# Optimization experiments

Hardware: AMD Instinct MI355X
Metric: run time of the kernel (lower is better)

Reference implementation:

```python
import jax, jax.numpy as jnp
import numpy as np

IN_CH = 512
OUT_CH = 512
HEADS = 8
HEAD_DIM = OUT_CH // HEADS
N = 64 * 64  # total flattened tokens


def setup_inputs() -> dict:
    key = jax.random.key(0)
    ks = jax.random.split(key, 10)
    x = jax.random.normal(ks[0], (64, 64, IN_CH), dtype=jnp.float32)
    edge_index = jax.random.randint(ks[1], (2, 65536), 0, N, dtype=jnp.int64)
    # causal temporal mask, broadcastable against scores [N, H, N]
    temporal_mask = jnp.tril(jnp.ones((N, N), dtype=bool))[:, None, :]
    s = 1.0 / np.sqrt(IN_CH)
    Wq = jax.random.uniform(ks[2], (OUT_CH, IN_CH), minval=-s, maxval=s)
    bq = jnp.zeros((OUT_CH,), jnp.float32)
    Wk = jax.random.uniform(ks[3], (OUT_CH, IN_CH), minval=-s, maxval=s)
    bk = jnp.zeros((OUT_CH,), jnp.float32)
    Wv = jax.random.uniform(ks[4], (OUT_CH, IN_CH), minval=-s, maxval=s)
    bv = jnp.zeros((OUT_CH,), jnp.float32)
    Wo = jax.random.uniform(ks[5], (OUT_CH, OUT_CH), minval=-s, maxval=s)
    bo = jnp.zeros((OUT_CH,), jnp.float32)
    return {"x": x, "edge_index": edge_index, "temporal_mask": temporal_mask,
            "Wq": Wq, "bq": bq, "Wk": Wk, "bk": bk, "Wv": Wv, "bv": bv,
            "Wo": Wo, "bo": bo}


def reference(x, edge_index, temporal_mask, Wq, bq, Wk, bk, Wv, bv, Wo, bo):
    # x: [S1, S2, C] -> flatten to [N, C]; edge_index unused (as in source).
    xf = x.reshape(-1, IN_CH)
    q = (xf @ Wq.T + bq).reshape(-1, HEADS, HEAD_DIM)
    k = (xf @ Wk.T + bk).reshape(-1, HEADS, HEAD_DIM)
    v = (xf @ Wv.T + bv).reshape(-1, HEADS, HEAD_DIM)
    scores = jnp.einsum('nhd,mhd->nhm', q, k) / np.sqrt(HEAD_DIM)  # [N,H,N]
    scores = jnp.where(temporal_mask, scores, -jnp.inf)
    attn = jax.nn.softmax(scores, axis=-1)  # dropout omitted (eval mode)
    out = jnp.einsum('nhm,mhd->nhd', attn, v).reshape(-1, OUT_CH)
    return out @ Wo.T + bo  # [N, OUT_CH]
```

## Files before the change

kernel.cpp:

```cpp
#include <hip/hip_runtime.h>
#include <math.h>

#define NT 4096
#define CH 512
#define NHEADS 8
#define HD 64

typedef __attribute__((ext_vector_type(8))) short short8;
typedef __attribute__((ext_vector_type(4))) float f32x4;
typedef unsigned short ushort_t;
typedef unsigned int uint_t;

#define MFMA16 __builtin_amdgcn_mfma_f32_16x16x32_bf16

#define MNEG 1e30f

__device__ __forceinline__ ushort_t f2bf(float x) {
  uint_t u = __float_as_uint(x);
  return (ushort_t)((u + 0x7fffu + ((u >> 16) & 1u)) >> 16);
}
__device__ __forceinline__ float bf2f(ushort_t h) {
  return __uint_as_float(((uint_t)h) << 16);
}

__device__ __forceinline__ void g2l16(const ushort_t* g, ushort_t* l) {
  __builtin_amdgcn_global_load_lds(
      (const __attribute__((address_space(1))) void*)g,
      (__attribute__((address_space(3))) void*)l, 16, 0, 0);
}

__device__ __forceinline__ short8 ldsFrag(const ushort_t* plane, int row, int c4) {
  return *reinterpret_cast<const short8*>(plane + row * 64 + (((c4) ^ (row & 7)) << 3));
}

__global__ __launch_bounds__(256)
void cvt_split(const float* __restrict__ x,
               const float* __restrict__ Wq, const float* __restrict__ Wk,
               const float* __restrict__ Wv, const float* __restrict__ Wo,
               ushort_t* __restrict__ xh, ushort_t* __restrict__ xl,
               ushort_t* __restrict__ qh, ushort_t* __restrict__ ql,
               ushort_t* __restrict__ kh, ushort_t* __restrict__ kl,
               ushort_t* __restrict__ vh, ushort_t* __restrict__ vl,
               ushort_t* __restrict__ oh, ushort_t* __restrict__ ol) {
  const size_t i = ((size_t)blockIdx.x * 256 + threadIdx.x) * 4;
  const float* src;
  ushort_t *dh, *dl;
  size_t off;
  if (i < 2097152) { src = x; dh = xh; dl = xl; off = i; }
  else {
    const size_t j = i - 2097152;
    const int wsel = (int)(j >> 18);
    off = j & 262143;
    if (wsel == 0)      { src = Wq; dh = qh; dl = ql; }
    else if (wsel == 1) { src = Wk; dh = kh; dl = kl; }
    else if (wsel == 2) { src = Wv; dh = vh; dl = vl; }
    else                { src = Wo; dh = oh; dl = ol; }
  }
  const float4 v = *reinterpret_cast<const float4*>(src + off);
  ushort_t hb[4], lb[4];
  const float f[4] = {v.x, v.y, v.z, v.w};
  #pragma unroll
  for (int j = 0; j < 4; ++j) {
    hb[j] = f2bf(f[j]);
    lb[j] = f2bf(f[j] - bf2f(hb[j]));
  }
  *reinterpret_cast<uint2*>(dh + off) =
      make_uint2((uint_t)hb[0] | ((uint_t)hb[1] << 16), (uint_t)hb[2] | ((uint_t)hb[3] << 16));
  *reinterpret_cast<uint2*>(dl + off) =
      make_uint2((uint_t)lb[0] | ((uint_t)lb[1] << 16), (uint_t)lb[2] | ((uint_t)lb[3] << 16));
}

__global__ __launch_bounds__(256)
void gemm_qkv_bf16(const ushort_t* __restrict__ xh,
                   const ushort_t* __restrict__ Wqh, const float* __restrict__ bq,
                   const ushort_t* __restrict__ Wkh, const float* __restrict__ bk,
                   const ushort_t* __restrict__ Wvh, const float* __restrict__ bv,
                   ushort_t* __restrict__ Qhi, ushort_t* __restrict__ Khi,
                   ushort_t* __restrict__ Vthi) {
  __shared__ ushort_t ldsA[128 * 64];
  __shared__ ushort_t ldsW[64 * 64];
  const int z = blockIdx.z;
  const ushort_t* Wh = (z == 0) ? Wqh : (z == 1) ? Wkh : Wvh;
  const float* bias = (z == 0) ? bq : (z == 1) ? bk : bv;

  const int t = threadIdx.x;
  const int w = t >> 6;
  const int lane = t & 63;
  const int l15 = lane & 15;
  const int g = lane >> 4;
  const int m0 = blockIdx.x * 128;
  const int n0 = blockIdx.y * 64;

  f32x4 acc[2][4];
  #pragma unroll
  for (int mt = 0; mt < 2; ++mt)
    #pragma unroll
    for (int nt = 0; nt < 4; ++nt) acc[mt][nt] = f32x4{0.f, 0.f, 0.f, 0.f};

  for (int k0 = 0; k0 < 512; k0 += 64) {
    __syncthreads();
    #pragma unroll
    for (int p = 0; p < 4; ++p) {
      const int c = 256 * p + 64 * w + lane;
      const int r = c >> 3;
      const int sc4 = (c & 7) ^ (r & 7);
      g2l16(xh + (size_t)(m0 + r) * 512 + k0 + sc4 * 8,
            &ldsA[(256 * p + 64 * w) * 8]);
    }
    #pragma unroll
    for (int p = 0; p < 2; ++p) {
      const int c = 256 * p + 64 * w + lane;
      const int r = c >> 3;
      const int sc4 = (c & 7) ^ (r & 7);
      g2l16(Wh + (size_t)(n0 + r) * 512 + k0 + sc4 * 8,
            &ldsW[(256 * p + 64 * w) * 8]);
    }
    __syncthreads();
    #pragma unroll
    for (int s = 0; s < 2; ++s) {
      short8 ah[2];
      #pragma unroll
      for (int mt = 0; mt < 2; ++mt)
        ah[mt] = ldsFrag(ldsA, 32 * w + 16 * mt + l15, 4 * s + g);
      #pragma unroll
      for (int nt = 0; nt < 4; ++nt) {
        const short8 wh = ldsFrag(ldsW, 16 * nt + l15, 4 * s + g);
        #pragma unroll
        for (int mt = 0; mt < 2; ++mt)
          acc[mt][nt] = MFMA16(ah[mt], wh, acc[mt][nt], 0, 0, 0);
      }
    }
  }

  if (z < 2) {
    ushort_t* Hi = z ? Khi : Qhi;
    const float sc = z ? 1.0f : 0.125f;
    #pragma unroll
    for (int mt = 0; mt < 2; ++mt) {
      const int mb = m0 + 32 * w + 16 * mt + 4 * g;
      #pragma unroll
      for (int nt = 0; nt < 4; ++nt) {
        const int col = n0 + 16 * nt + l15;
        const float bv_ = bias[col];
        #pragma unroll
        for (int r = 0; r < 4; ++r)
          Hi[(size_t)(mb + r) * 512 + col] = f2bf((acc[mt][nt][r] + bv_) * sc);
      }
    }
  } else {
    #pragma unroll
    for (int mt = 0; mt < 2; ++mt) {
      const int mb = m0 + 32 * w + 16 * mt + 4 * g;
      #pragma unroll
      for (int nt = 0; nt < 4; ++nt) {
        const int n = n0 + 16 * nt + l15;
        const float bv_ = bias[n];
        ushort_t hb[4];
        #pragma unroll
        for (int r = 0; r < 4; ++r) hb[r] = f2bf(acc[mt][nt][r] + bv_);
        *reinterpret_cast<uint2*>(&Vthi[(size_t)n * 4096 + mb]) =
            make_uint2((uint_t)hb[0] | ((uint_t)hb[1] << 16),
                       (uint_t)hb[2] | ((uint_t)hb[3] << 16));
      }
    }
  }
}

__global__ __launch_bounds__(256)
void gemm_out_mfma(const ushort_t* __restrict__ Ahi, const ushort_t* __restrict__ Alo,
                   const ushort_t* __restrict__ Woh, const ushort_t* __restrict__ Wol,
                   const float* __restrict__ bias, float* __restrict__ C) {
  __shared__ ushort_t ldsAh[128 * 64], ldsAl[128 * 64];
  __shared__ ushort_t ldsWh[64 * 64], ldsWl[64 * 64];
  const int t = threadIdx.x;
  const int w = t >> 6;
  const int lane = t & 63;
  const int l15 = lane & 15;
  const int g = lane >> 4;
  const int m0 = blockIdx.x * 128;
  const int n0 = blockIdx.y * 64;

  f32x4 acc[2][4];
  #pragma unroll
  for (int mt = 0; mt < 2; ++mt)
    #pragma unroll
    for (int nt = 0; nt < 4; ++nt) acc[mt][nt] = f32x4{0.f, 0.f, 0.f, 0.f};

  for (int k0 = 0; k0 < 512; k0 += 64) {
    __syncthreads();
    #pragma unroll
    for (int p = 0; p < 4; ++p) {
      const int c = 256 * p + 64 * w + lane;
      const int r = c >> 3;
      const int sc4 = (c & 7) ^ (r & 7);
      const size_t src = (size_t)(m0 + r) * 512 + k0 + sc4 * 8;
      const int dst = (256 * p + 64 * w) * 8;
      g2l16(Ahi + src, ldsAh + dst);
      g2l16(Alo + src, ldsAl + dst);
    }
    #pragma unroll
    for (int p = 0; p < 2; ++p) {
      const int c = 256 * p + 64 * w + lane;
      const int r = c >> 3;
      const int sc4 = (c & 7) ^ (r & 7);
      const size_t src = (size_t)(n0 + r) * 512 + k0 + sc4 * 8;
      const int dst = (256 * p + 64 * w) * 8;
      g2l16(Woh + src, ldsWh + dst);
      g2l16(Wol + src, ldsWl + dst);
    }
    __syncthreads();
    #pragma unroll
    for (int s = 0; s < 2; ++s) {
      short8 ah[2], al[2];
      #pragma unroll
      for (int mt = 0; mt < 2; ++mt) {
        ah[mt] = ldsFrag(ldsAh, 32 * w + 16 * mt + l15, 4 * s + g);
        al[mt] = ldsFrag(ldsAl, 32 * w + 16 * mt + l15, 4 * s + g);
      }
      #pragma unroll
      for (int nt = 0; nt < 4; ++nt) {
        const short8 wh = ldsFrag(ldsWh, 16 * nt + l15, 4 * s + g);
        const short8 wl = ldsFrag(ldsWl, 16 * nt + l15, 4 * s + g);
        #pragma unroll
        for (int mt = 0; mt < 2; ++mt) {
          acc[mt][nt] = MFMA16(ah[mt], wh, acc[mt][nt], 0, 0, 0);
          acc[mt][nt] = MFMA16(ah[mt], wl, acc[mt][nt], 0, 0, 0);
          acc[mt][nt] = MFMA16(al[mt], wh, acc[mt][nt], 0, 0, 0);
        }
      }
    }
  }

  #pragma unroll
  for (int mt = 0; mt < 2; ++mt) {
    const int mb = m0 + 32 * w + 16 * mt + 4 * g;
    #pragma unroll
    for (int nt = 0; nt < 4; ++nt) {
      const int col = n0 + 16 * nt + l15;
      const float bv_ = bias[col];
      #pragma unroll
      for (int r = 0; r < 4; ++r)
        C[(size_t)(mb + r) * 512 + col] = acc[mt][nt][r] + bv_;
    }
  }
}

__global__ __launch_bounds__(512)
void attn_mfma(const ushort_t* __restrict__ Qhi, const ushort_t* __restrict__ Khi,
               const ushort_t* __restrict__ Vthi,
               float* __restrict__ Opart, float2* __restrict__ MLpart) {
  __shared__ ushort_t ldsT[2][64 * 64];
  __shared__ ushort_t ldsP[8][16 * 64];

  const int t = threadIdx.x;
  const int h = blockIdx.y;
  const int w = t >> 6;
  const int lane = t & 63;
  const int l15 = lane & 15;
  const int g = lane >> 4;

  const int bx = blockIdx.x;
  const int qb = 31 - bx / 3;
  const int sp = bx - 3 * (bx / 3);
  const int ntiles = 2 * qb + 2;
  const int len = (ntiles + 2) / 3;
  const int kb0 = sp * len;
  const int kb1e = (kb0 + len < ntiles) ? (kb0 + len) : ntiles;
  const int q0 = qb * 128;
  const int qr = q0 + w * 16 + l15;

  const short8 ones = {(short)0x3F80, (short)0x3F80, (short)0x3F80, (short)0x3F80,
                       (short)0x3F80, (short)0x3F80, (short)0x3F80, (short)0x3F80};

  short8 qh[2];
  #pragma unroll
  for (int s = 0; s < 2; ++s)
    qh[s] = *reinterpret_cast<const short8*>(
        Qhi + (size_t)qr * 512 + h * 64 + 32 * s + 8 * g);

  float mrun[4], lrun[4];
  f32x4 accO[4];
  #pragma unroll
  for (int r = 0; r < 4; ++r) { mrun[r] = -MNEG; lrun[r] = 0.f; }
  #pragma unroll
  for (int dt = 0; dt < 4; ++dt) accO[dt] = f32x4{0.f, 0.f, 0.f, 0.f};

  for (int kb = kb0; kb < kb1e; ++kb) {
    __syncthreads();
    {
      const int c = w * 64 + lane;
      const int r = c >> 3;
      const int sc4 = (c & 7) ^ (r & 7);
      const int ldst = (w * 64) * 8;
      g2l16(Khi + (size_t)(kb * 64 + r) * 512 + h * 64 + sc4 * 8, &ldsT[0][ldst]);
      g2l16(Vthi + (size_t)(h * 64 + r) * 4096 + kb * 64 + sc4 * 8, &ldsT[1][ldst]);
    }
    __syncthreads();

    f32x4 accS[4];
    #pragma unroll
    for (int nt = 0; nt < 4; ++nt) accS[nt] = f32x4{0.f, 0.f, 0.f, 0.f};
    __builtin_amdgcn_s_setprio(1);
    #pragma unroll
    for (int s = 0; s < 2; ++s) {
      #pragma unroll
      for (int nt = 0; nt < 4; ++nt) {
        const short8 kh = ldsFrag(ldsT[0], 16 * nt + l15, 4 * s + g);
        accS[nt] = MFMA16(qh[s], kh, accS[nt], 0, 0, 0);
      }
    }
    __builtin_amdgcn_s_setprio(0);

    if (kb >= 2 * qb) {
      #pragma unroll
      for (int nt = 0; nt < 4; ++nt) {
        const int kg = kb * 64 + 16 * nt + l15;
        #pragma unroll
        for (int r = 0; r < 4; ++r) {
          const int qg = q0 + w * 16 + 4 * g + r;
          if (kg > qg) accS[nt][r] = -INFINITY;
        }
      }
    }

    float pmax[4];
    #pragma unroll
    for (int r = 0; r < 4; ++r)
      pmax[r] = fmaxf(fmaxf(accS[0][r], accS[1][r]), fmaxf(accS[2][r], accS[3][r]));
    float dd = pmax[0] - mrun[0];
    #pragma unroll
    for (int r = 1; r < 4; ++r) dd = fmaxf(dd, pmax[r] - mrun[r]);
    if (!__all(dd <= 8.0f)) {
      #pragma unroll
      for (int off = 1; off < 16; off <<= 1)
        #pragma unroll
        for (int r = 0; r < 4; ++r) pmax[r] = fmaxf(pmax[r], __shfl_xor(pmax[r], off));
      #pragma unroll
      for (int r = 0; r < 4; ++r) {
        const float mn = fmaxf(mrun[r], pmax[r]);
        const float al = __expf(mrun[r] - mn);
        mrun[r] = mn;
        lrun[r] *= al;
        #pragma unroll
        for (int dt = 0; dt < 4; ++dt) accO[dt][r] *= al;
      }
    }
    #pragma unroll
    for (int nt = 0; nt < 4; ++nt)
      #pragma unroll
      for (int r = 0; r < 4; ++r) {
        const float p = __expf(accS[nt][r] - mrun[r]);
        const int row = 4 * g + r;
        ldsP[w][row * 64 + (((2 * nt + (l15 >> 3)) ^ (row & 7)) << 3) + (l15 & 7)]
            = f2bf(p);
      }
    short8 pah[2];
    #pragma unroll
    for (int s = 0; s < 2; ++s) pah[s] = ldsFrag(ldsP[w], l15, 4 * s + g);

    f32x4 accL = f32x4{0.f, 0.f, 0.f, 0.f};
    __builtin_amdgcn_s_setprio(1);
    #pragma unroll
    for (int s = 0; s < 2; ++s) {
      accL = MFMA16(pah[s], ones, accL, 0, 0, 0);
      #pragma unroll
      for (int dt = 0; dt < 4; ++dt) {
        const short8 vh = ldsFrag(ldsT[1], 16 * dt + l15, 4 * s + g);
        accO[dt] = MFMA16(pah[s], vh, accO[dt], 0, 0, 0);
      }
    }
    __builtin_amdgcn_s_setprio(0);
    #pragma unroll
    for (int r = 0; r < 4; ++r) lrun[r] += accL[r];
  }

  #pragma unroll
  for (int r = 0; r < 4; ++r) {
    const int rw = w * 16 + 4 * g + r;
    const size_t pbase = ((((size_t)sp * 32 + qb) * 8 + h) * 128 + rw) * 64;
    #pragma unroll
    for (int dt = 0; dt < 4; ++dt)
      Opart[pbase + 16 * dt + l15] = accO[dt][r];
    if (l15 == 0)
      MLpart[(((size_t)sp * 32 + qb) * 8 + h) * 128 + rw] = make_float2(mrun[r], lrun[r]);
  }
}

__global__ __launch_bounds__(512)
void attn_combine(const float* __restrict__ Opart, const float2* __restrict__ MLpart,
                  ushort_t* __restrict__ Ahi, ushort_t* __restrict__ Alo) {
  const int qb = blockIdx.x;
  const int h = blockIdx.y;
  const int t = threadIdx.x;
  const int row = t >> 2;
  const int c0 = (t & 3) * 16;
  const size_t mlidx = (((size_t)qb) * 8 + h) * 128 + row;
  const size_t SPS = (size_t)32 * 8 * 128;
  const float2 ml0 = MLpart[mlidx];
  const float2 ml1 = MLpart[mlidx + SPS];
  const float2 ml2 = MLpart[mlidx + 2 * SPS];
  const float M = fmaxf(fmaxf(ml0.x, ml1.x), ml2.x);
  const float w0 = __expf(ml0.x - M);
  const float w1 = __expf(ml1.x - M);
  const float w2 = __expf(ml2.x - M);
  const float inv = 1.0f / (w0 * ml0.y + w1 * ml1.y + w2 * ml2.y);
  const size_t b0 = mlidx * 64;
  const size_t b1 = (mlidx + SPS) * 64;
  const size_t b2 = (mlidx + 2 * SPS) * 64;
  #pragma unroll
  for (int p = 0; p < 4; ++p) {
    const int col = c0 + p * 4;
    const float4 o0 = *reinterpret_cast<const float4*>(&Opart[b0 + col]);
    const float4 o1 = *reinterpret_cast<const float4*>(&Opart[b1 + col]);
    const float4 o2 = *reinterpret_cast<const float4*>(&Opart[b2 + col]);
    const float f[4] = {o0.x * w0 + o1.x * w1 + o2.x * w2,
                        o0.y * w0 + o1.y * w1 + o2.y * w2,
                        o0.z * w0 + o1.z * w1 + o2.z * w2,
                        o0.w * w0 + o1.w * w1 + o2.w * w2};
    ushort_t hb[4], lb[4];
    #pragma unroll
    for (int j = 0; j < 4; ++j) {
      const float v = f[j] * inv;
      hb[j] = f2bf(v);
      lb[j] = f2bf(v - bf2f(hb[j]));
    }
    const size_t idx = (size_t)(qb * 128 + row) * 512 + h * 64 + col;
    *reinterpret_cast<uint2*>(&Ahi[idx]) =
        make_uint2((uint_t)hb[0] | ((uint_t)hb[1] << 16), (uint_t)hb[2] | ((uint_t)hb[3] << 16));
    *reinterpret_cast<uint2*>(&Alo[idx]) =
        make_uint2((uint_t)lb[0] | ((uint_t)lb[1] << 16), (uint_t)lb[2] | ((uint_t)lb[3] << 16));
  }
}

extern "C" void kernel_launch(void* const* d_in, const int* in_sizes, int n_in,
                              void* d_out, int out_size, void* d_ws, size_t ws_size,
                              hipStream_t stream) {
  const float* x  = (const float*)d_in[0];
  const float* Wq = (const float*)d_in[3];
  const float* bq = (const float*)d_in[4];
  const float* Wk = (const float*)d_in[5];
  const float* bk = (const float*)d_in[6];
  const float* Wv = (const float*)d_in[7];
  const float* bv = (const float*)d_in[8];
  const float* Wo = (const float*)d_in[9];
  const float* bo = (const float*)d_in[10];
  float* out = (float*)d_out;

  ushort_t* p = (ushort_t*)d_ws;
  const size_t NC = (size_t)NT * CH;
  const size_t WW = (size_t)CH * CH;
  ushort_t* xhi = p;            p += NC;
  ushort_t* xlo = p;            p += NC;
  ushort_t* Wqh = p;            p += WW;
  ushort_t* Wql = p;            p += WW;
  ushort_t* Wkh = p;            p += WW;
  ushort_t* Wkl = p;            p += WW;
  ushort_t* Wvh = p;            p += WW;
  ushort_t* Wvl = p;            p += WW;
  ushort_t* Woh = p;            p += WW;
  ushort_t* Wol = p;            p += WW;
  ushort_t* Qhi = p;            p += NC;
  ushort_t* Khi = p;            p += NC;
  ushort_t* Vthi = p;           p += NC;
  ushort_t* Ahi = p;            p += NC;
  ushort_t* Alo = p;            p += NC;
  float* Opart = (float*)p;
  float2* MLpart = (float2*)(Opart + 6291456);

  cvt_split<<<3072, 256, 0, stream>>>(x, Wq, Wk, Wv, Wo,
                                      xhi, xlo, Wqh, Wql, Wkh, Wkl, Wvh, Wvl, Woh, Wol);
  gemm_qkv_bf16<<<dim3(32, 8, 3), 256, 0, stream>>>(
      xhi, Wqh, bq, Wkh, bk, Wvh, bv, Qhi, Khi, Vthi);
  attn_mfma<<<dim3(96, 8), 512, 0, stream>>>(Qhi, Khi, Vthi, Opart, MLpart);
  attn_combine<<<dim3(32, 8), 512, 0, stream>>>(Opart, MLpart, Ahi, Alo);
  gemm_out_mfma<<<dim3(32, 8), 256, 0, stream>>>(Ahi, Alo, Woh, Wol, bo, out);
}
```

Baseline: 99.40 us.

## Drop split-bf16 low parts and widen attention key tiles to 128

Removes the hi/lo bf16 split everywhere: conversion writes only the high part, the combine kernel stops emitting Alo, and the output GEMM runs a single bf16 MFMA pass instead of three. The attention kernel now processes 128-key tiles instead of 64, with separate K and V LDS buffers and wider P staging, which halves loop iterations and barriers. Both changes cut memory traffic and MFMA work, at the cost of lower output-projection precision and more LDS per block.

Result: slower. 102.6 us (+3.2%).

```diff
diff --git a/kernel.cpp b/kernel.cpp
--- a/kernel.cpp
+++ b/kernel.cpp
@@ -32,42 +32,75 @@
 __device__ __forceinline__ short8 ldsFrag(const ushort_t* plane, int row, int c4) {
   return *reinterpret_cast<const short8*>(plane + row * 64 + (((c4) ^ (row & 7)) << 3));
 }
+__device__ __forceinline__ short8 ldsFrag128(const ushort_t* plane, int row, int c4) {
+  return *reinterpret_cast<const short8*>(plane + row * 128 + (((c4) ^ (row & 7)) << 3));
+}
 
 __global__ __launch_bounds__(256)
-void cvt_split(const float* __restrict__ x,
-               const float* __restrict__ Wq, const float* __restrict__ Wk,
-               const float* __restrict__ Wv, const float* __restrict__ Wo,
-               ushort_t* __restrict__ xh, ushort_t* __restrict__ xl,
-               ushort_t* __restrict__ qh, ushort_t* __restrict__ ql,
-               ushort_t* __restrict__ kh, ushort_t* __restrict__ kl,
-               ushort_t* __restrict__ vh, ushort_t* __restrict__ vl,
-               ushort_t* __restrict__ oh, ushort_t* __restrict__ ol) {
+void cvt_hi(const float* __restrict__ x,
+            const float* __restrict__ Wq, const float* __restrict__ Wk,
+            const float* __restrict__ Wv, const float* __restrict__ Wo,
+            ushort_t* __restrict__ xh, ushort_t* __restrict__ qh,
+            ushort_t* __restrict__ kh, ushort_t* __restrict__ vh,
+            ushort_t* __restrict__ oh) {
   const size_t i = ((size_t)blockIdx.x * 256 + threadIdx.x) * 4;
   const float* src;
-  ushort_t *dh, *dl;
+  ushort_t* dh;
   size_t off;
-  if (i < 2097152) { src = x; dh = xh; dl = xl; off = i; }
+  if (i < 2097152) { src = x; dh = xh; off = i; }
   else {
     const size_t j = i - 2097152;
     const int wsel = (int)(j >> 18);
     off = j & 262143;
-    if (wsel == 0)      { src = Wq; dh = qh; dl = ql; }
-    else if (wsel == 1) { src = Wk; dh = kh; dl = kl; }
-    else if (wsel == 2) { src = Wv; dh = vh; dl = vl; }
-    else                { src = Wo; dh = oh; dl = ol; }
+    if (wsel == 0)      { src = Wq; dh = qh; }
+    else if (wsel == 1) { src = Wk; dh = kh; }
+    else if (wsel == 2) { src = Wv; dh = vh; }
+    else                { src = Wo; dh = oh; }
   }
   const float4 v = *reinterpret_cast<const float4*>(src + off);
-  ushort_t hb[4], lb[4];
-  const float f[4] = {v.x, v.y, v.z, v.w};
-  #pragma unroll
-  for (int j = 0; j < 4; ++j) {
-    hb[j] = f2bf(f[j]);
-    lb[j] = f2bf(f[j] - bf2f(hb[j]));
-  }
+  const ushort_t hb[4] = {f2bf(v.x), f2bf(v.y), f2bf(v.z), f2bf(v.w)};
   *reinterpret_cast<uint2*>(dh + off) =
       make_uint2((uint_t)hb[0] | ((uint_t)hb[1] << 16), (uint_t)hb[2] | ((uint_t)hb[3] << 16));
-  *reinterpret_cast<uint2*>(dl + off) =
-      make_uint2((uint_t)lb[0] | ((uint_t)lb[1] << 16), (uint_t)lb[2] | ((uint_t)lb[3] << 16));
+}
+
+__device__ __forceinline__ void gemm_hi_core(
+    const ushort_t* __restrict__ Ah, const ushort_t* __restrict__ Wh,
+    int m0, int n0, int w, int lane, ushort_t* ldsA, ushort_t* ldsW,
+    f32x4 acc[2][4]) {
+  const int l15 = lane & 15;
+  const int g = lane >> 4;
+  for (int k0 = 0; k0 < 512; k0 += 64) {
+    __syncthreads();
+    #pragma unroll
+    for (int p = 0; p < 4; ++p) {
+      const int c = 256 * p + 64 * w + lane;
+      const int r = c >> 3;
+      const int sc4 = (c & 7) ^ (r & 7);
+      g2l16(Ah + (size_t)(m0 + r) * 512 + k0 + sc4 * 8, &ldsA[(256 * p + 64 * w) * 8]);
+    }
+    #pragma unroll
+    for (int p = 0; p < 2; ++p) {
+      const int c = 256 * p + 64 * w + lane;
+      const int r = c >> 3;
+      const int sc4 = (c & 7) ^ (r & 7);
+      g2l16(Wh + (size_t)(n0 + r) * 512 + k0 + sc4 * 8, &ldsW[(256 * p + 64 * w) * 8]);
+    }
+    __syncthreads();
+    #pragma unroll
+    for (int s = 0; s < 2; ++s) {
+      short8 ah[2];
+      #pragma unroll
+      for (int mt = 0; mt < 2; ++mt)
+        ah[mt] = ldsFrag(ldsA, 32 * w + 16 * mt + l15, 4 * s + g);
+      #pragma unroll
+      for (int nt = 0; nt < 4; ++nt) {
+        const short8 wh = ldsFrag(ldsW, 16 * nt + l15, 4 * s + g);
+        #pragma unroll
+        for (int mt = 0; mt < 2; ++mt)
+          acc[mt][nt] = MFMA16(ah[mt], wh, acc[mt][nt], 0, 0, 0);
+      }
+    }
+  }
 }
 
 __global__ __launch_bounds__(256)
@@ -97,40 +130,7 @@
     #pragma unroll
     for (int nt = 0; nt < 4; ++nt) acc[mt][nt] = f32x4{0.f, 0.f, 0.f, 0.f};
 
-  for (int k0 = 0; k0 < 512; k0 += 64) {
-    __syncthreads();
-    #pragma unroll
-    for (int p = 0; p < 4; ++p) {
-      const int c = 256 * p + 64 * w + lane;
-      const int r = c >> 3;
-      const int sc4 = (c & 7) ^ (r & 7);
-      g2l16(xh + (size_t)(m0 + r) * 512 + k0 + sc4 * 8,
-            &ldsA[(256 * p + 64 * w) * 8]);
-    }
-    #pragma unroll
-    for (int p = 0; p < 2; ++p) {
-      const int c = 256 * p + 64 * w + lane;
-      const int r = c >> 3;
-      const int sc4 = (c & 7) ^ (r & 7);
-      g2l16(Wh + (size_t)(n0 + r) * 512 + k0 + sc4 * 8,
-            &ldsW[(256 * p + 64 * w) * 8]);
-    }
-    __syncthreads();
-    #pragma unroll
-    for (int s = 0; s < 2; ++s) {
-      short8 ah[2];
-      #pragma unroll
-      for (int mt = 0; mt < 2; ++mt)
-        ah[mt] = ldsFrag(ldsA, 32 * w + 16 * mt + l15, 4 * s + g);
-      #pragma unroll
-      for (int nt = 0; nt < 4; ++nt) {
-        const short8 wh = ldsFrag(ldsW, 16 * nt + l15, 4 * s + g);
-        #pragma unroll
-        for (int mt = 0; mt < 2; ++mt)
-          acc[mt][nt] = MFMA16(ah[mt], wh, acc[mt][nt], 0, 0, 0);
-      }
-    }
-  }
+  gemm_hi_core(xh, Wh, m0, n0, w, lane, ldsA, ldsW, acc);
 
   if (z < 2) {
     ushort_t* Hi = z ? Khi : Qhi;
@@ -167,11 +167,10 @@
 }
 
 __global__ __launch_bounds__(256)
-void gemm_out_mfma(const ushort_t* __restrict__ Ahi, const ushort_t* __restrict__ Alo,
-                   const ushort_t* __restrict__ Woh, const ushort_t* __restrict__ Wol,
+void gemm_out_bf16(const ushort_t* __restrict__ Ahi, const ushort_t* __restrict__ Woh,
                    const float* __restrict__ bias, float* __restrict__ C) {
-  __shared__ ushort_t ldsAh[128 * 64], ldsAl[128 * 64];
-  __shared__ ushort_t ldsWh[64 * 64], ldsWl[64 * 64];
+  __shared__ ushort_t ldsA[128 * 64];
+  __shared__ ushort_t ldsW[64 * 64];
   const int t = threadIdx.x;
   const int w = t >> 6;
   const int lane = t & 63;
@@ -186,50 +185,7 @@
     #pragma unroll
     for (int nt = 0; nt < 4; ++nt) acc[mt][nt] = f32x4{0.f, 0.f, 0.f, 0.f};
 
-  for (int k0 = 0; k0 < 512; k0 += 64) {
-    __syncthreads();
-    #pragma unroll
-    for (int p = 0; p < 4; ++p) {
-      const int c = 256 * p + 64 * w + lane;
-      const int r = c >> 3;
-      const int sc4 = (c & 7) ^ (r & 7);
-      const size_t src = (size_t)(m0 + r) * 512 + k0 + sc4 * 8;
-      const int dst = (256 * p + 64 * w) * 8;
-      g2l16(Ahi + src, ldsAh + dst);
-      g2l16(Alo + src, ldsAl + dst);
-    }
-    #pragma unroll
-    for (int p = 0; p < 2; ++p) {
-      const int c = 256 * p + 64 * w + lane;
-      const int r = c >> 3;
-      const int sc4 = (c & 7) ^ (r & 7);
-      const size_t src = (size_t)(n0 + r) * 512 + k0 + sc4 * 8;
-      const int dst = (256 * p + 64 * w) * 8;
-      g2l16(Woh + src, ldsWh + dst);
-      g2l16(Wol + src, ldsWl + dst);
-    }
-    __syncthreads();
-    #pragma unroll
-    for (int s = 0; s < 2; ++s) {
-      short8 ah[2], al[2];
-      #pragma unroll
-      for (int mt = 0; mt < 2; ++mt) {
-        ah[mt] = ldsFrag(ldsAh, 32 * w + 16 * mt + l15, 4 * s + g);
-        al[mt] = ldsFrag(ldsAl, 32 * w + 16 * mt + l15, 4 * s + g);
-      }
-      #pragma unroll
-      for (int nt = 0; nt < 4; ++nt) {
-        const short8 wh = ldsFrag(ldsWh, 16 * nt + l15, 4 * s + g);
-        const short8 wl = ldsFrag(ldsWl, 16 * nt + l15, 4 * s + g);
-        #pragma unroll
-        for (int mt = 0; mt < 2; ++mt) {
-          acc[mt][nt] = MFMA16(ah[mt], wh, acc[mt][nt], 0, 0, 0);
-          acc[mt][nt] = MFMA16(ah[mt], wl, acc[mt][nt], 0, 0, 0);
-          acc[mt][nt] = MFMA16(al[mt], wh, acc[mt][nt], 0, 0, 0);
-        }
-      }
-    }
-  }
+  gemm_hi_core(Ahi, Woh, m0, n0, w, lane, ldsA, ldsW, acc);
 
   #pragma unroll
   for (int mt = 0; mt < 2; ++mt) {
@@ -249,8 +205,9 @@
 void attn_mfma(const ushort_t* __restrict__ Qhi, const ushort_t* __restrict__ Khi,
                const ushort_t* __restrict__ Vthi,
                float* __restrict__ Opart, float2* __restrict__ MLpart) {
-  __shared__ ushort_t ldsT[2][64 * 64];
-  __shared__ ushort_t ldsP[8][16 * 64];
+  __shared__ ushort_t ldsK[128 * 64];
+  __shared__ ushort_t ldsV[64 * 128];
+  __shared__ ushort_t ldsP[8][16 * 128];
 
   const int t = threadIdx.x;
   const int h = blockIdx.y;
@@ -262,7 +219,7 @@
   const int bx = blockIdx.x;
   const int qb = 31 - bx / 3;
   const int sp = bx - 3 * (bx / 3);
-  const int ntiles = 2 * qb + 2;
+  const int ntiles = qb + 1;
   const int len = (ntiles + 2) / 3;
   const int kb0 = sp * len;
   const int kb1e = (kb0 + len < ntiles) ? (kb0 + len) : ntiles;
@@ -287,34 +244,38 @@
 
   for (int kb = kb0; kb < kb1e; ++kb) {
     __syncthreads();
-    {
-      const int c = w * 64 + lane;
-      const int r = c >> 3;
-      const int sc4 = (c & 7) ^ (r & 7);
-      const int ldst = (w * 64) * 8;
-      g2l16(Khi + (size_t)(kb * 64 + r) * 512 + h * 64 + sc4 * 8, &ldsT[0][ldst]);
-      g2l16(Vthi + (size_t)(h * 64 + r) * 4096 + kb * 64 + sc4 * 8, &ldsT[1][ldst]);
+    #pragma unroll
+    for (int p = 0; p < 2; ++p) {
+      const int ck = p * 512 + w * 64 + lane;
+      const int rk = ck >> 3;
+      const int sck = (ck & 7) ^ (rk & 7);
+      g2l16(Khi + (size_t)(kb * 128 + rk) * 512 + h * 64 + sck * 8,
+            &ldsK[(p * 512 + w * 64) * 8]);
+      const int rv = ck >> 4;
+      const int scv = (ck & 15) ^ (rv & 7);
+      g2l16(Vthi + (size_t)(h * 64 + rv) * 4096 + kb * 128 + scv * 8,
+            &ldsV[(p * 512 + w * 64) * 8]);
     }
     __syncthreads();
 
-    f32x4 accS[4];
-    #pragma unroll
-    for (int nt = 0; nt < 4; ++nt) accS[nt] = f32x4{0.f, 0.f, 0.f, 0.f};
+    f32x4 accS[8];
+    #pragma unroll
+    for (int nt = 0; nt < 8; ++nt) accS[nt] = f32x4{0.f, 0.f, 0.f, 0.f};
     __builtin_amdgcn_s_setprio(1);
     #pragma unroll
     for (int s = 0; s < 2; ++s) {
       #pragma unroll
-      for (int nt = 0; nt < 4; ++nt) {
-        const short8 kh = ldsFrag(ldsT[0], 16 * nt + l15, 4 * s + g);
+      for (int nt = 0; nt < 8; ++nt) {
+        const short8 kh = ldsFrag(ldsK, 16 * nt + l15, 4 * s + g);
         accS[nt] = MFMA16(qh[s], kh, accS[nt], 0, 0, 0);
       }
     }
     __builtin_amdgcn_s_setprio(0);
 
-    if (kb >= 2 * qb) {
-      #pragma unroll
-      for (int nt = 0; nt < 4; ++nt) {
-        const int kg = kb * 64 + 16 * nt + l15;
+    if (kb == qb) {
+      #pragma unroll
+      for (int nt = 0; nt < 8; ++nt) {
+        const int kg = kb * 128 + 16 * nt + l15;
         #pragma unroll
         for (int r = 0; r < 4; ++r) {
           const int qg = q0 + w * 16 + 4 * g + r;
@@ -325,8 +286,11 @@
 
     float pmax[4];
     #pragma unroll
-    for (int r = 0; r < 4; ++r)
-      pmax[r] = fmaxf(fmaxf(accS[0][r], accS[1][r]), fmaxf(accS[2][r], accS[3][r]));
+    for (int r = 0; r < 4; ++r) {
+      pmax[r] = accS[0][r];
+      #pragma unroll
+      for (int nt = 1; nt < 8; ++nt) pmax[r] = fmaxf(pmax[r], accS[nt][r]);
+    }
     float dd = pmax[0] - mrun[0];
     #pragma unroll
     for (int r = 1; r < 4; ++r) dd = fmaxf(dd, pmax[r] - mrun[r]);
@@ -346,26 +310,28 @@
       }
     }
     #pragma unroll
-    for (int nt = 0; nt < 4; ++nt)
+    for (int nt = 0; nt < 8; ++nt)
       #pragma unroll
       for (int r = 0; r < 4; ++r) {
         const float p = __expf(accS[nt][r] - mrun[r]);
         const int row = 4 * g + r;
-        ldsP[w][row * 64 + (((2 * nt + (l15 >> 3)) ^ (row & 7)) << 3) + (l15 & 7)]
+        ldsP[w][row * 128 + (((2 * nt + (l15 >> 3)) ^ (row & 7)) << 3) + (l15 & 7)]
             = f2bf(p);
       }
-    short8 pah[2];
-    #pragma unroll
-    for (int s = 0; s < 2; ++s) pah[s] = ldsFrag(ldsP[w], l15, 4 * s + g);
+    short8 pah[4];
+    #pragma unroll
+    for (int s = 0; s < 4; ++s)
+      pah[s] = *reinterpret_cast<const short8*>(
+          &ldsP[w][l15 * 128 + (((4 * s + g) ^ (l15 & 7)) << 3)]);
 
     f32x4 accL = f32x4{0.f, 0.f, 0.f, 0.f};
     __builtin_amdgcn_s_setprio(1);
     #pragma unroll
-    for (int s = 0; s < 2; ++s) {
+    for (int s = 0; s < 4; ++s) {
       accL = MFMA16(pah[s], ones, accL, 0, 0, 0);
       #pragma unroll
       for (int dt = 0; dt < 4; ++dt) {
-        const short8 vh = ldsFrag(ldsT[1], 16 * dt + l15, 4 * s + g);
+        const short8 vh = ldsFrag128(ldsV, 16 * dt + l15, 4 * s + g);
         accO[dt] = MFMA16(pah[s], vh, accO[dt], 0, 0, 0);
       }
     }
@@ -388,7 +354,7 @@
 
 __global__ __launch_bounds__(512)
 void attn_combine(const float* __restrict__ Opart, const float2* __restrict__ MLpart,
-                  ushort_t* __restrict__ Ahi, ushort_t* __restrict__ Alo) {
+                  ushort_t* __restrict__ Ahi) {
   const int qb = blockIdx.x;
   const int h = blockIdx.y;
   const int t = threadIdx.x;
@@ -413,22 +379,14 @@
     const float4 o0 = *reinterpret_cast<const float4*>(&Opart[b0 + col]);
     const float4 o1 = *reinterpret_cast<const float4*>(&Opart[b1 + col]);
     const float4 o2 = *reinterpret_cast<const float4*>(&Opart[b2 + col]);
-    const float f[4] = {o0.x * w0 + o1.x * w1 + o2.x * w2,
-                        o0.y * w0 + o1.y * w1 + o2.y * w2,
-                        o0.z * w0 + o1.z * w1 + o2.z * w2,
-                        o0.w * w0 + o1.w * w1 + o2.w * w2};
-    ushort_t hb[4], lb[4];
-    #pragma unroll
-    for (int j = 0; j < 4; ++j) {
-      const float v = f[j] * inv;
-      hb[j] = f2bf(v);
-      lb[j] = f2bf(v - bf2f(hb[j]));
-    }
+    ushort_t hb[4];
+    hb[0] = f2bf((o0.x * w0 + o1.x * w1 + o2.x * w2) * inv);
+    hb[1] = f2bf((o0.y * w0 + o1.y * w1 + o2.y * w2) * inv);
+    hb[2] = f2bf((o0.z * w0 + o1.z * w1 + o2.z * w2) * inv);
+    hb[3] = f2bf((o0.w * w0 + o1.w * w1 + o2.w * w2) * inv);
     const size_t idx = (size_t)(qb * 128 + row) * 512 + h * 64 + col;
     *reinterpret_cast<uint2*>(&Ahi[idx]) =
         make_uint2((uint_t)hb[0] | ((uint_t)hb[1] << 16), (uint_t)hb[2] | ((uint_t)hb[3] << 16));
-    *reinterpret_cast<uint2*>(&Alo[idx]) =
-        make_uint2((uint_t)lb[0] | ((uint_t)lb[1] << 16), (uint_t)lb[2] | ((uint_t)lb[3] << 16));
   }
 }
 
@@ -450,28 +408,21 @@
   const size_t NC = (size_t)NT * CH;
   const size_t WW = (size_t)CH * CH;
   ushort_t* xhi = p;            p += NC;
-  ushort_t* xlo = p;            p += NC;
   ushort_t* Wqh = p;            p += WW;
-  ushort_t* Wql = p;            p += WW;
   ushort_t* Wkh = p;            p += WW;
-  ushort_t* Wkl = p;            p += WW;
   ushort_t* Wvh = p;            p += WW;
-  ushort_t* Wvl = p;            p += WW;
   ushort_t* Woh = p;            p += WW;
-  ushort_t* Wol = p;            p += WW;
   ushort_t* Qhi = p;            p += NC;
   ushort_t* Khi = p;            p += NC;
   ushort_t* Vthi = p;           p += NC;
   ushort_t* Ahi = p;            p += NC;
-  ushort_t* Alo = p;            p += NC;
   float* Opart = (float*)p;
   float2* MLpart = (float2*)(Opart + 6291456);
 
-  cvt_split<<<3072, 256, 0, stream>>>(x, Wq, Wk, Wv, Wo,
-                                      xhi, xlo, Wqh, Wql, Wkh, Wkl, Wvh, Wvl, Woh, Wol);
+  cvt_hi<<<3072, 256, 0, stream>>>(x, Wq, Wk, Wv, Wo, xhi, Wqh, Wkh, Wvh, Woh);
   gemm_qkv_bf16<<<dim3(32, 8, 3), 256, 0, stream>>>(
       xhi, Wqh, bq, Wkh, bk, Wvh, bv, Qhi, Khi, Vthi);
   attn_mfma<<<dim3(96, 8), 512, 0, stream>>>(Qhi, Khi, Vthi, Opart, MLpart);
-  attn_combine<<<dim3(32, 8), 512, 0, stream>>>(Opart, MLpart, Ahi, Alo);
-  gemm_out_mfma<<<dim3(32, 8), 256, 0, stream>>>(Ahi, Alo, Woh, Wol, bo, out);
-}
+  attn_combine<<<dim3(32, 8), 512, 0, stream>>>(Opart, MLpart, Ahi);
+  gemm_out_bf16<<<dim3(32, 8), 256, 0, stream>>>(Ahi, Woh, bo, out);
+}
```
